# Kernel optimization log

Measured on AMD Instinct MI355X. Metric: run time of the kernel, lower is better.

The kernel has to match this reference:

```python
import jax, jax.numpy as jnp
import numpy as np

N, F, H, T = 100000, 128, 128, 10
E = 1600000
NUM_GRAPHS = 512
BN_EPS = 1e-5


def setup_inputs() -> dict:
    key = jax.random.key(0)
    ks = jax.random.split(key, 16)
    x = jax.random.normal(ks[0], (N, F), dtype=jnp.float32)
    edge_index = jax.random.randint(ks[1], (2, E), 0, N, dtype=jnp.int64)
    batch = jnp.sort(jax.random.randint(ks[2], (N,), 0, NUM_GRAPHS, dtype=jnp.int64))
    s = lambda fin: 1.0 / np.sqrt(fin)
    return {
        "x": x, "edge_index": edge_index, "batch": batch,
        # GINConv 1 MLP: Linear(F,H) -> BN(H) -> ReLU -> Linear(H,H)
        "W1a": jax.random.uniform(ks[3], (F, H), jnp.float32, -s(F), s(F)),
        "b1a": jax.random.uniform(ks[4], (H,), jnp.float32, -s(F), s(F)),
        "g1": jnp.ones((H,), jnp.float32),
        "bt1": jnp.zeros((H,), jnp.float32),
        "W1b": jax.random.uniform(ks[5], (H, H), jnp.float32, -s(H), s(H)),
        "b1b": jax.random.uniform(ks[6], (H,), jnp.float32, -s(H), s(H)),
        # GINConv 2 MLP
        "W2a": jax.random.uniform(ks[7], (H, H), jnp.float32, -s(H), s(H)),
        "b2a": jax.random.uniform(ks[8], (H,), jnp.float32, -s(H), s(H)),
        "g2": jnp.ones((H,), jnp.float32),
        "bt2": jnp.zeros((H,), jnp.float32),
        "W2b": jax.random.uniform(ks[9], (H, H), jnp.float32, -s(H), s(H)),
        "b2b": jax.random.uniform(ks[10], (H,), jnp.float32, -s(H), s(H)),
        # final Linear(H, T)
        "Wl": jax.random.uniform(ks[11], (H, T), jnp.float32, -s(H), s(H)),
        "bl": jax.random.uniform(ks[12], (T,), jnp.float32, -s(H), s(H)),
    }


def _batchnorm(h, gamma, beta):
    # training-mode BN over the node dimension (biased variance), eps=1e-5
    mean = jnp.mean(h, axis=0)
    var = jnp.mean(jnp.square(h - mean), axis=0)
    return (h - mean) * jax.lax.rsqrt(var + BN_EPS) * gamma + beta


def _gin_conv(x, edge_index, Wa, ba, gamma, beta, Wb, bb):
    src, dst = edge_index[0], edge_index[1]
    # sum-aggregate neighbor messages: scatter-add x[src] into dst rows
    agg = jax.ops.segment_sum(x[src], dst, num_segments=x.shape[0])
    h = (x + agg) @ Wa + ba          # eps=0 in GINConv default
    h = jax.nn.relu(_batchnorm(h, gamma, beta))
    return h @ Wb + bb


def reference(x, edge_index, batch, W1a, b1a, g1, bt1, W1b, b1b,
              W2a, b2a, g2, bt2, W2b, b2b, Wl, bl):
    h = jax.nn.relu(_gin_conv(x, edge_index, W1a, b1a, g1, bt1, W1b, b1b))
    h = jax.nn.relu(_gin_conv(h, edge_index, W2a, b2a, g2, bt2, W2b, b2b))
    pooled = jax.ops.segment_sum(h, batch, num_segments=NUM_GRAPHS)  # [G, H]
    return pooled @ Wl + bl  # [G, T]
```

## Files before the change

### kernel.cpp

```cpp
#include <hip/hip_runtime.h>
#include <cstdint>
#include <cstddef>

#define NFEAT 128
#define TGRAPH 10
#define NGRAPHS 512
#define BN_EPS 1e-5f
#define BIN_CHUNK 2048

typedef __attribute__((ext_vector_type(8))) short bf16x8;
typedef __attribute__((ext_vector_type(4))) float f32x4;

__device__ __forceinline__ float bf2f(short s) {
    union { unsigned u; float f; } c;
    c.u = ((unsigned)(unsigned short)s) << 16;
    return c.f;
}
__device__ __forceinline__ short f2bf(float f) {
    union { float f; unsigned u; } c;
    c.f = f;
    unsigned u = c.u;
    return (short)((u + 0x7fffu + ((u >> 16) & 1u)) >> 16);
}

__global__ __launch_bounds__(256) void k_bucket_hist(const int* __restrict__ dst,
                                                     int* __restrict__ bhist, int E) {
    __shared__ int h[256];
    int t = threadIdx.x;
    h[t] = 0;
    __syncthreads();
    for (int e = blockIdx.x * blockDim.x + t; e < E; e += gridDim.x * blockDim.x)
        atomicAdd(&h[dst[e] >> 9], 1);
    __syncthreads();
    if (h[t]) atomicAdd(&bhist[t], h[t]);
}

__global__ void k_bucket_scan(const int* __restrict__ bhist, int* __restrict__ bbase,
                              int* __restrict__ cur256, int E) {
    __shared__ int s[256];
    int t = threadIdx.x;
    int v = bhist[t];
    s[t] = v;
    __syncthreads();
    for (int off = 1; off < 256; off <<= 1) {
        int x = 0;
        if (t >= off) x = s[t - off];
        __syncthreads();
        if (t >= off) s[t] += x;
        __syncthreads();
    }
    int excl = s[t] - v;
    bbase[t] = excl;
    cur256[t] = excl;
    if (t == 255) bbase[256] = E;
}

__global__ __launch_bounds__(256) void k_bin_scatter(const int* __restrict__ src,
                                                     const int* __restrict__ dst,
                                                     int* __restrict__ cur256,
                                                     int2* __restrict__ binned, int E) {
    __shared__ int hist[256];
    __shared__ int base[256];
    int t = threadIdx.x;
    int e0 = blockIdx.x * BIN_CHUNK;
    int e1 = min(e0 + BIN_CHUNK, E);
    hist[t] = 0;
    __syncthreads();
    for (int e = e0 + t; e < e1; e += 256) {
        int b = dst[e] >> 9;
        atomicAdd(&hist[b], 1);
    }
    __syncthreads();
    int c = hist[t];
    if (c > 0) base[t] = atomicAdd(&cur256[t], c);
    __syncthreads();
    hist[t] = 0;
    __syncthreads();
    for (int e = e0 + t; e < e1; e += 256) {
        int d = dst[e];
        int b = d >> 9;
        int loc = atomicAdd(&hist[b], 1);
        binned[base[b] + loc] = make_int2(src[e], d);
    }
}

__global__ __launch_bounds__(512) void k_bucket_csr(const int2* __restrict__ binned,
                                                    const int* __restrict__ bbase,
                                                    int* __restrict__ rowptr,
                                                    int* __restrict__ adj,
                                                    int N, int E, int nb) {
    __shared__ int deg[512];
    __shared__ int cur[512];
    int b = blockIdx.x;
    int t = threadIdx.x;
    int e0 = bbase[b], e1 = bbase[b + 1];
    deg[t] = 0;
    __syncthreads();
    for (int e = e0 + t; e < e1; e += 512)
        atomicAdd(&deg[binned[e].y & 511], 1);
    __syncthreads();
    int v = deg[t];
    for (int off = 1; off < 512; off <<= 1) {
        int x = 0;
        if (t >= off) x = deg[t - off];
        __syncthreads();
        if (t >= off) deg[t] += x;
        __syncthreads();
    }
    int excl = deg[t] - v;
    cur[t] = excl;
    int node = b * 512 + t;
    if (node < N) rowptr[node] = e0 + excl;
    if (b == nb - 1 && t == 0) rowptr[N] = E;
    __syncthreads();
    for (int e = e0 + t; e < e1; e += 512) {
        int2 p = binned[e];
        int loc = atomicAdd(&cur[p.y & 511], 1);
        adj[e0 + loc] = p.x;
    }
}

__global__ void k_prep(const float* __restrict__ x, short* __restrict__ xbf,
                       const float* __restrict__ W0, const float* __restrict__ W1,
                       const float* __restrict__ W2, const float* __restrict__ W3,
                       short* __restrict__ Wf, int n4) {
    int i = blockIdx.x * blockDim.x + threadIdx.x;
    if (i < n4) {
        float4 v = ((const float4*)x)[i];
        ushort4 o;
        o.x = (unsigned short)f2bf(v.x);
        o.y = (unsigned short)f2bf(v.y);
        o.z = (unsigned short)f2bf(v.z);
        o.w = (unsigned short)f2bf(v.w);
        ((ushort4*)xbf)[i] = o;
    } else {
        int idx = i - n4;
        if (idx < 4 * 16384) {
            int w = idx >> 14, r = idx & 16383;
            int j = r & 7, lane = (r >> 3) & 63, ct = (r >> 9) & 7, kc = r >> 12;
            int k = kc * 32 + (lane >> 4) * 8 + j;
            int n = ct * 16 + (lane & 15);
            const float* W = (w == 0) ? W0 : (w == 1) ? W1 : (w == 2) ? W2 : W3;
            Wf[idx] = f2bf(W[k * NFEAT + n]);
        }
    }
}

__global__ __launch_bounds__(256) void k_aggregate_bf(const short* __restrict__ X,
                                                      const int* __restrict__ rowptr,
                                                      const int* __restrict__ adj,
                                                      short* __restrict__ XA, int N) {
    int lane = threadIdx.x & 63;
    int wid = (blockIdx.x * blockDim.x + threadIdx.x) >> 6;
    int nw = (gridDim.x * blockDim.x) >> 6;
    for (; wid < N; wid += nw) {
        unsigned sv = *(const unsigned*)(X + (size_t)wid * NFEAT + lane * 2);
        float ax = bf2f((short)(sv & 0xffff));
        float ay = bf2f((short)(sv >> 16));
        int e = rowptr[wid], r1 = rowptr[wid + 1];
        for (; e + 8 <= r1; e += 8) {
            int s[8];
#pragma unroll
            for (int j = 0; j < 8; j++) s[j] = adj[e + j];
            unsigned v[8];
#pragma unroll
            for (int j = 0; j < 8; j++)
                v[j] = *(const unsigned*)(X + (size_t)s[j] * NFEAT + lane * 2);
#pragma unroll
            for (int j = 0; j < 8; j++) {
                ax += bf2f((short)(v[j] & 0xffff));
                ay += bf2f((short)(v[j] >> 16));
            }
        }
        for (; e < r1; ++e) {
            int s0 = adj[e];
            unsigned v0 = *(const unsigned*)(X + (size_t)s0 * NFEAT + lane * 2);
            ax += bf2f((short)(v0 & 0xffff));
            ay += bf2f((short)(v0 >> 16));
        }
        unsigned o = (unsigned)(unsigned short)f2bf(ax) | ((unsigned)(unsigned short)f2bf(ay) << 16);
        *(unsigned*)(XA + (size_t)wid * NFEAT + lane * 2) = o;
    }
}

template <bool BN_RELU_IN, bool RELU_OUT, bool STATS>
__global__ __launch_bounds__(256) void k_gemm_mfma(const short* __restrict__ A,
                                                   const short* __restrict__ Wf,
                                                   const float* __restrict__ bias,
                                                   const float* __restrict__ scale,
                                                   const float* __restrict__ shift,
                                                   float* __restrict__ stats,
                                                   short* __restrict__ C, int N) {
    __shared__ float s_sum[NFEAT];
    __shared__ float s_sq[NFEAT];
    int tid = threadIdx.x;
    int wave = tid >> 6, lane = tid & 63;
    int quad = lane >> 4, l16 = lane & 15;
    int row_base = blockIdx.x * 128 + wave * 32;

    if constexpr (STATS) {
        if (tid < NFEAT) { s_sum[tid] = 0.f; s_sq[tid] = 0.f; }
        __syncthreads();
    }

    f32x4 acc[2][8];
#pragma unroll
    for (int i = 0; i < 2; i++)
#pragma unroll
        for (int j = 0; j < 8; j++) acc[i][j] = (f32x4){0.f, 0.f, 0.f, 0.f};

    int r0 = row_base + l16;
    int r1 = r0 + 16;

#pragma unroll
    for (int kc = 0; kc < 4; ++kc) {
        int koff = kc * 32 + quad * 8;
        bf16x8 a0 = {}, a1 = {};
        if (r0 < N) a0 = *(const bf16x8*)(A + (size_t)r0 * NFEAT + koff);
        if (r1 < N) a1 = *(const bf16x8*)(A + (size_t)r1 * NFEAT + koff);
        if constexpr (BN_RELU_IN) {
            float sc[8], sh[8];
            *(float4*)(sc) = *(const float4*)(scale + koff);
            *(float4*)(sc + 4) = *(const float4*)(scale + koff + 4);
            *(float4*)(sh) = *(const float4*)(shift + koff);
            *(float4*)(sh + 4) = *(const float4*)(shift + koff + 4);
#pragma unroll
            for (int j = 0; j < 8; j++) {
                float v = fmaxf(bf2f(a0[j]) * sc[j] + sh[j], 0.f);
                float u = fmaxf(bf2f(a1[j]) * sc[j] + sh[j], 0.f);
                a0[j] = f2bf(v);
                a1[j] = f2bf(u);
            }
        }
        const short* wp = Wf + ((size_t)(kc * 8) * 64 + lane) * 8;
#pragma unroll
        for (int ct = 0; ct < 8; ++ct) {
            bf16x8 b = *(const bf16x8*)(wp + (size_t)ct * 64 * 8);
            acc[0][ct] = __builtin_amdgcn_mfma_f32_16x16x32_bf16(a0, b, acc[0][ct], 0, 0, 0);
            acc[1][ct] = __builtin_amdgcn_mfma_f32_16x16x32_bf16(a1, b, acc[1][ct], 0, 0, 0);
        }
    }

#pragma unroll
    for (int ct = 0; ct < 8; ++ct) {
        int col = ct * 16 + l16;
        float bv = bias[col];
        float ls = 0.f, ls2 = 0.f;
#pragma unroll
        for (int rt = 0; rt < 2; ++rt) {
#pragma unroll
            for (int reg = 0; reg < 4; ++reg) {
                int row = row_base + rt * 16 + quad * 4 + reg;
                if (row < N) {
                    float v = acc[rt][ct][reg] + bv;
                    if constexpr (RELU_OUT) v = fmaxf(v, 0.f);
                    C[(size_t)row * NFEAT + col] = f2bf(v);
                    if constexpr (STATS) { ls += v; ls2 += v * v; }
                }
            }
        }
        if constexpr (STATS) {
            atomicAdd(&s_sum[col], ls);
            atomicAdd(&s_sq[col], ls2);
        }
    }

    if constexpr (STATS) {
        __syncthreads();
        if (tid < NFEAT) {
            atomicAdd(&stats[tid], s_sum[tid]);
            atomicAdd(&stats[NFEAT + tid], s_sq[tid]);
        }
    }
}

__global__ void k_bnfinalize(const float* __restrict__ stats, const float* __restrict__ gamma,
                             const float* __restrict__ beta, float* __restrict__ scale,
                             float* __restrict__ shift, int N) {
    int c = threadIdx.x;
    if (c < NFEAT) {
        float mean = stats[c] / (float)N;
        float var = stats[NFEAT + c] / (float)N - mean * mean;
        float inv = rsqrtf(var + BN_EPS);
        float sc = gamma[c] * inv;
        scale[c] = sc;
        shift[c] = beta[c] - mean * sc;
    }
}

__global__ __launch_bounds__(256) void k_pool2(const short* __restrict__ H2,
                                               const int* __restrict__ batch,
                                               float* __restrict__ pooled, int N) {
    int t = threadIdx.x;
    int c2 = t & 63;
    int rofs = t >> 6;
    int n0 = blockIdx.x * 128;
    int cur = -1;
    float ax = 0.f, ay = 0.f;
    for (int i = 0; i < 32; ++i) {
        int n = n0 + rofs + i * 4;
        if (n >= N) break;
        int g = batch[n];
        if (g != cur) {
            if (cur >= 0) {
                atomicAdd(&pooled[cur * NFEAT + c2 * 2], ax);
                atomicAdd(&pooled[cur * NFEAT + c2 * 2 + 1], ay);
            }
            cur = g; ax = 0.f; ay = 0.f;
        }
        unsigned v = *(const unsigned*)(H2 + (size_t)n * NFEAT + c2 * 2);
        ax += bf2f((short)(v & 0xffff));
        ay += bf2f((short)(v >> 16));
    }
    if (cur >= 0) {
        atomicAdd(&pooled[cur * NFEAT + c2 * 2], ax);
        atomicAdd(&pooled[cur * NFEAT + c2 * 2 + 1], ay);
    }
}

__global__ void k_final(const float* __restrict__ pooled, const float* __restrict__ Wl,
                        const float* __restrict__ bl, float* __restrict__ out) {
    int idx = blockIdx.x * blockDim.x + threadIdx.x;
    if (idx >= NGRAPHS * TGRAPH) return;
    int g = idx / TGRAPH, t = idx % TGRAPH;
    const float* p = pooled + (size_t)g * NFEAT;
    float acc = bl[t];
#pragma unroll 16
    for (int k = 0; k < NFEAT; ++k) acc += p[k] * Wl[k * TGRAPH + t];
    out[idx] = acc;
}

extern "C" void kernel_launch(void* const* d_in, const int* in_sizes, int n_in,
                              void* d_out, int out_size, void* d_ws, size_t ws_size,
                              hipStream_t stream) {
    const float* x = (const float*)d_in[0];
    const int* ei = (const int*)d_in[1];
    const int* batch = (const int*)d_in[2];
    const float* W1a = (const float*)d_in[3];
    const float* b1a = (const float*)d_in[4];
    const float* g1 = (const float*)d_in[5];
    const float* bt1 = (const float*)d_in[6];
    const float* W1b = (const float*)d_in[7];
    const float* b1b = (const float*)d_in[8];
    const float* W2a = (const float*)d_in[9];
    const float* b2a = (const float*)d_in[10];
    const float* g2 = (const float*)d_in[11];
    const float* bt2 = (const float*)d_in[12];
    const float* W2b = (const float*)d_in[13];
    const float* b2b = (const float*)d_in[14];
    const float* Wl = (const float*)d_in[15];
    const float* bl = (const float*)d_in[16];
    float* out = (float*)d_out;

    int N = in_sizes[2];
    int E = in_sizes[1] / 2;
    int nb = (N + 511) >> 9;
    const int* src = ei;
    const int* dst = ei + E;

    char* ws = (char*)d_ws;
    size_t off = 0;
    auto alloc = [&](size_t bytes) -> void* {
        void* p = ws + off;
        off = (off + bytes + 255) & ~(size_t)255;
        return p;
    };
    short* xbf = (short*)alloc((size_t)N * NFEAT * 2);
    short* ag = (short*)alloc((size_t)N * NFEAT * 2);
    short* ybf = (short*)alloc((size_t)N * NFEAT * 2);
    short* hbf = (short*)alloc((size_t)N * NFEAT * 2);
    short* h2bf = (short*)alloc((size_t)N * NFEAT * 2);
    short* Wf = (short*)alloc((size_t)4 * 16384 * 2);
    int* adj = (int*)alloc((size_t)E * 4);
    int2* binned = (int2*)alloc((size_t)E * 8);
    int* rowptr = (int*)alloc((size_t)(N + 1) * 4);
    int* bbase = (int*)alloc(257 * 4);
    int* cur256 = (int*)alloc(256 * 4);
    float* scale = (float*)alloc(128 * 4);
    float* shift = (float*)alloc(128 * 4);
    int* bhist = (int*)alloc(256 * 4);
    float* stats1 = (float*)alloc(256 * 4);
    float* stats2 = (float*)alloc(256 * 4);
    float* pooled = (float*)alloc((size_t)NGRAPHS * NFEAT * 4);
    size_t zbytes = (char*)(pooled + (size_t)NGRAPHS * NFEAT) - (char*)bhist;

    hipMemsetAsync(bhist, 0, zbytes, stream);

    k_bucket_hist<<<784, 256, 0, stream>>>(dst, bhist, E);
    k_bucket_scan<<<1, 256, 0, stream>>>(bhist, bbase, cur256, E);
    k_bin_scatter<<<(E + BIN_CHUNK - 1) / BIN_CHUNK, 256, 0, stream>>>(src, dst, cur256, binned, E);
    k_bucket_csr<<<nb, 512, 0, stream>>>(binned, bbase, rowptr, adj, N, E, nb);

    int n4 = N * NFEAT / 4;
    int prepTot = n4 + 4 * 16384;
    k_prep<<<(prepTot + 255) / 256, 256, 0, stream>>>(x, xbf, W1a, W1b, W2a, W2b, Wf, n4);

    int gemmBlocks = (N + 127) / 128;

    k_aggregate_bf<<<2048, 256, 0, stream>>>(xbf, rowptr, adj, ag, N);
    k_gemm_mfma<false, false, true><<<gemmBlocks, 256, 0, stream>>>(ag, Wf + 0 * 16384, b1a, nullptr, nullptr, stats1, ybf, N);
    k_bnfinalize<<<1, 128, 0, stream>>>(stats1, g1, bt1, scale, shift, N);
    k_gemm_mfma<true, true, false><<<gemmBlocks, 256, 0, stream>>>(ybf, Wf + 1 * 16384, b1b, scale, shift, nullptr, hbf, N);

    k_aggregate_bf<<<2048, 256, 0, stream>>>(hbf, rowptr, adj, ag, N);
    k_gemm_mfma<false, false, true><<<gemmBlocks, 256, 0, stream>>>(ag, Wf + 2 * 16384, b2a, nullptr, nullptr, stats2, ybf, N);
    k_bnfinalize<<<1, 128, 0, stream>>>(stats2, g2, bt2, scale, shift, N);
    k_gemm_mfma<true, true, false><<<gemmBlocks, 256, 0, stream>>>(ybf, Wf + 3 * 16384, b2b, scale, shift, nullptr, h2bf, N);

    k_pool2<<<(N + 127) / 128, 256, 0, stream>>>(h2bf, batch, pooled, N);
    k_final<<<(NGRAPHS * TGRAPH + 255) / 256, 256, 0, stream>>>(pooled, Wl, bl, out);
}
```

Baseline: 537.0 us.

## Slice feature columns across blocks and parallelize neighbor edges within a wave

Rewrites the neighbor aggregation so each block handles one 32-byte slice of the feature row, and each wave splits its lanes into 8 edge slots by 8 feature lanes. Neighbor partial sums are then combined with cross-lane shuffles. This is meant to raise memory-level parallelism per node and to improve cache locality, since each block only touches one eighth of the feature matrix. The cost is 8x redundant rowptr/adj reads and narrow 32-byte gathers per edge, plus idle slots on nodes with few neighbors.

After: 916.6 us. 70.7% more time.

```diff
diff --git a/kernel.cpp b/kernel.cpp
--- a/kernel.cpp
+++ b/kernel.cpp
@@ -146,40 +146,46 @@
     }
 }
 
-__global__ __launch_bounds__(256) void k_aggregate_bf(const short* __restrict__ X,
+__global__ __launch_bounds__(256) void k_aggregate_sl(const short* __restrict__ X,
                                                       const int* __restrict__ rowptr,
                                                       const int* __restrict__ adj,
                                                       short* __restrict__ XA, int N) {
-    int lane = threadIdx.x & 63;
-    int wid = (blockIdx.x * blockDim.x + threadIdx.x) >> 6;
-    int nw = (gridDim.x * blockDim.x) >> 6;
-    for (; wid < N; wid += nw) {
-        unsigned sv = *(const unsigned*)(X + (size_t)wid * NFEAT + lane * 2);
-        float ax = bf2f((short)(sv & 0xffff));
-        float ay = bf2f((short)(sv >> 16));
-        int e = rowptr[wid], r1 = rowptr[wid + 1];
-        for (; e + 8 <= r1; e += 8) {
-            int s[8];
-#pragma unroll
-            for (int j = 0; j < 8; j++) s[j] = adj[e + j];
-            unsigned v[8];
-#pragma unroll
-            for (int j = 0; j < 8; j++)
-                v[j] = *(const unsigned*)(X + (size_t)s[j] * NFEAT + lane * 2);
-#pragma unroll
-            for (int j = 0; j < 8; j++) {
-                ax += bf2f((short)(v[j] & 0xffff));
-                ay += bf2f((short)(v[j] >> 16));
+    int tid = threadIdx.x;
+    int lane = tid & 63;
+    int slot = lane >> 3;
+    int d = lane & 7;
+    int slice = blockIdx.x & 7;
+    int sliceByte = slice * 32 + d * 4;
+    int wid = (blockIdx.x >> 3) * 4 + (tid >> 6);
+    int nw = (gridDim.x >> 3) * 4;
+    const char* Xb = (const char*)X;
+    for (int n = wid; n < N; n += nw) {
+        int r0 = rowptr[n], r1 = rowptr[n + 1];
+        float ax = 0.f, ay = 0.f;
+        for (int e = r0; e < r1; e += 8) {
+            int ee = e + slot;
+            unsigned v = 0;
+            if (ee < r1) {
+                int srow = adj[ee];
+                v = *(const unsigned*)(Xb + (size_t)srow * 256 + sliceByte);
             }
-        }
-        for (; e < r1; ++e) {
-            int s0 = adj[e];
-            unsigned v0 = *(const unsigned*)(X + (size_t)s0 * NFEAT + lane * 2);
-            ax += bf2f((short)(v0 & 0xffff));
-            ay += bf2f((short)(v0 >> 16));
-        }
-        unsigned o = (unsigned)(unsigned short)f2bf(ax) | ((unsigned)(unsigned short)f2bf(ay) << 16);
-        *(unsigned*)(XA + (size_t)wid * NFEAT + lane * 2) = o;
+            ax += bf2f((short)(v & 0xffff));
+            ay += bf2f((short)(v >> 16));
+        }
+        ax += __shfl_xor(ax, 8);
+        ay += __shfl_xor(ay, 8);
+        ax += __shfl_xor(ax, 16);
+        ay += __shfl_xor(ay, 16);
+        ax += __shfl_xor(ax, 32);
+        ay += __shfl_xor(ay, 32);
+        if (slot == 0) {
+            unsigned sv = *(const unsigned*)(Xb + (size_t)n * 256 + sliceByte);
+            ax += bf2f((short)(sv & 0xffff));
+            ay += bf2f((short)(sv >> 16));
+            unsigned o = (unsigned)(unsigned short)f2bf(ax) |
+                         ((unsigned)(unsigned short)f2bf(ay) << 16);
+            *(unsigned*)((char*)XA + (size_t)n * 256 + sliceByte) = o;
+        }
     }
 }
 
@@ -396,13 +402,14 @@
     k_prep<<<(prepTot + 255) / 256, 256, 0, stream>>>(x, xbf, W1a, W1b, W2a, W2b, Wf, n4);
 
     int gemmBlocks = (N + 127) / 128;
-
-    k_aggregate_bf<<<2048, 256, 0, stream>>>(xbf, rowptr, adj, ag, N);
+    int aggBlocks = 8 * 512;
+
+    k_aggregate_sl<<<aggBlocks, 256, 0, stream>>>(xbf, rowptr, adj, ag, N);
     k_gemm_mfma<false, false, true><<<gemmBlocks, 256, 0, stream>>>(ag, Wf + 0 * 16384, b1a, nullptr, nullptr, stats1, ybf, N);
     k_bnfinalize<<<1, 128, 0, stream>>>(stats1, g1, bt1, scale, shift, N);
     k_gemm_mfma<true, true, false><<<gemmBlocks, 256, 0, stream>>>(ybf, Wf + 1 * 16384, b1b, scale, shift, nullptr, hbf, N);
 
-    k_aggregate_bf<<<2048, 256, 0, stream>>>(hbf, rowptr, adj, ag, N);
+    k_aggregate_sl<<<aggBlocks, 256, 0, stream>>>(hbf, rowptr, adj, ag, N);
     k_gemm_mfma<false, false, true><<<gemmBlocks, 256, 0, stream>>>(ag, Wf + 2 * 16384, b2a, nullptr, nullptr, stats2, ybf, N);
     k_bnfinalize<<<1, 128, 0, stream>>>(stats2, g2, bt2, scale, shift, N);
     k_gemm_mfma<true, true, false><<<gemmBlocks, 256, 0, stream>>>(ybf, Wf + 3 * 16384, b2b, scale, shift, nullptr, h2bf, N);
```

## Split each node's gather across four 16-lane groups with 16-byte loads

Applied to the files above, without the earlier changes.

The aggregation kernel now assigns four edge streams per wave. Each 16-lane group loads a full 256-byte bf16 row with uint4 loads, and partial sums are combined with cross-lane shuffles. It replaces the grid-stride loop with one wave per node and uses a cheaper bf16-to-float unpack. The goal is more independent loads in flight and wider memory transactions for the irregular neighbor gather. In exchange it uses more registers for the eight accumulators and adds shuffle overhead, and three quarters of the lanes sit idle during the final store.

Measured after the change: 530.6 us. No clear change (-1.2%).

```diff
diff --git a/kernel.cpp b/kernel.cpp
--- a/kernel.cpp
+++ b/kernel.cpp
@@ -21,6 +21,13 @@
     c.f = f;
     unsigned u = c.u;
     return (short)((u + 0x7fffu + ((u >> 16) & 1u)) >> 16);
+}
+__device__ __forceinline__ void acc2(float& a, float& b, unsigned v) {
+    union { unsigned u; float f; } lo, hi;
+    lo.u = v << 16;
+    hi.u = v & 0xffff0000u;
+    a += lo.f;
+    b += hi.f;
 }
 
 __global__ __launch_bounds__(256) void k_bucket_hist(const int* __restrict__ dst,
@@ -146,40 +153,52 @@
     }
 }
 
-__global__ __launch_bounds__(256) void k_aggregate_bf(const short* __restrict__ X,
+__global__ __launch_bounds__(256) void k_aggregate_v4(const short* __restrict__ X,
                                                       const int* __restrict__ rowptr,
                                                       const int* __restrict__ adj,
                                                       short* __restrict__ XA, int N) {
-    int lane = threadIdx.x & 63;
-    int wid = (blockIdx.x * blockDim.x + threadIdx.x) >> 6;
-    int nw = (gridDim.x * blockDim.x) >> 6;
-    for (; wid < N; wid += nw) {
-        unsigned sv = *(const unsigned*)(X + (size_t)wid * NFEAT + lane * 2);
-        float ax = bf2f((short)(sv & 0xffff));
-        float ay = bf2f((short)(sv >> 16));
-        int e = rowptr[wid], r1 = rowptr[wid + 1];
-        for (; e + 8 <= r1; e += 8) {
-            int s[8];
-#pragma unroll
-            for (int j = 0; j < 8; j++) s[j] = adj[e + j];
-            unsigned v[8];
-#pragma unroll
-            for (int j = 0; j < 8; j++)
-                v[j] = *(const unsigned*)(X + (size_t)s[j] * NFEAT + lane * 2);
-#pragma unroll
-            for (int j = 0; j < 8; j++) {
-                ax += bf2f((short)(v[j] & 0xffff));
-                ay += bf2f((short)(v[j] >> 16));
-            }
-        }
-        for (; e < r1; ++e) {
-            int s0 = adj[e];
-            unsigned v0 = *(const unsigned*)(X + (size_t)s0 * NFEAT + lane * 2);
-            ax += bf2f((short)(v0 & 0xffff));
-            ay += bf2f((short)(v0 >> 16));
-        }
-        unsigned o = (unsigned)(unsigned short)f2bf(ax) | ((unsigned)(unsigned short)f2bf(ay) << 16);
-        *(unsigned*)(XA + (size_t)wid * NFEAT + lane * 2) = o;
+    int tid = threadIdx.x;
+    int lane = tid & 63;
+    int g = lane >> 4;
+    int p = lane & 15;
+    int wid = (blockIdx.x * blockDim.x + tid) >> 6;
+    if (wid >= N) return;
+    const uint4* Xv = (const uint4*)X;
+    float acc[8];
+#pragma unroll
+    for (int j = 0; j < 8; j++) acc[j] = 0.f;
+    int r0 = rowptr[wid], r1 = rowptr[wid + 1];
+    for (int e = r0; e < r1; e += 8) {
+        int e0 = e + g, e1 = e + 4 + g;
+        uint4 v0 = {0u, 0u, 0u, 0u}, v1 = {0u, 0u, 0u, 0u};
+        if (e0 < r1) v0 = Xv[(size_t)adj[e0] * 16 + p];
+        if (e1 < r1) v1 = Xv[(size_t)adj[e1] * 16 + p];
+        acc2(acc[0], acc[1], v0.x);
+        acc2(acc[2], acc[3], v0.y);
+        acc2(acc[4], acc[5], v0.z);
+        acc2(acc[6], acc[7], v0.w);
+        acc2(acc[0], acc[1], v1.x);
+        acc2(acc[2], acc[3], v1.y);
+        acc2(acc[4], acc[5], v1.z);
+        acc2(acc[6], acc[7], v1.w);
+    }
+#pragma unroll
+    for (int j = 0; j < 8; j++) {
+        acc[j] += __shfl_xor(acc[j], 16);
+        acc[j] += __shfl_xor(acc[j], 32);
+    }
+    if (g == 0) {
+        uint4 sv = Xv[(size_t)wid * 16 + p];
+        acc2(acc[0], acc[1], sv.x);
+        acc2(acc[2], acc[3], sv.y);
+        acc2(acc[4], acc[5], sv.z);
+        acc2(acc[6], acc[7], sv.w);
+        uint4 o;
+        o.x = (unsigned)(unsigned short)f2bf(acc[0]) | ((unsigned)(unsigned short)f2bf(acc[1]) << 16);
+        o.y = (unsigned)(unsigned short)f2bf(acc[2]) | ((unsigned)(unsigned short)f2bf(acc[3]) << 16);
+        o.z = (unsigned)(unsigned short)f2bf(acc[4]) | ((unsigned)(unsigned short)f2bf(acc[5]) << 16);
+        o.w = (unsigned)(unsigned short)f2bf(acc[6]) | ((unsigned)(unsigned short)f2bf(acc[7]) << 16);
+        ((uint4*)XA)[(size_t)wid * 16 + p] = o;
     }
 }
 
@@ -396,13 +415,14 @@
     k_prep<<<(prepTot + 255) / 256, 256, 0, stream>>>(x, xbf, W1a, W1b, W2a, W2b, Wf, n4);
 
     int gemmBlocks = (N + 127) / 128;
-
-    k_aggregate_bf<<<2048, 256, 0, stream>>>(xbf, rowptr, adj, ag, N);
+    int aggBlocks = (N + 3) / 4;
+
+    k_aggregate_v4<<<aggBlocks, 256, 0, stream>>>(xbf, rowptr, adj, ag, N);
     k_gemm_mfma<false, false, true><<<gemmBlocks, 256, 0, stream>>>(ag, Wf + 0 * 16384, b1a, nullptr, nullptr, stats1, ybf, N);
     k_bnfinalize<<<1, 128, 0, stream>>>(stats1, g1, bt1, scale, shift, N);
     k_gemm_mfma<true, true, false><<<gemmBlocks, 256, 0, stream>>>(ybf, Wf + 1 * 16384, b1b, scale, shift, nullptr, hbf, N);
 
-    k_aggregate_bf<<<2048, 256, 0, stream>>>(hbf, rowptr, adj, ag, N);
+    k_aggregate_v4<<<aggBlocks, 256, 0, stream>>>(hbf, rowptr, adj, ag, N);
     k_gemm_mfma<false, false, true><<<gemmBlocks, 256, 0, stream>>>(ag, Wf + 2 * 16384, b2a, nullptr, nullptr, stats2, ybf, N);
     k_bnfinalize<<<1, 128, 0, stream>>>(stats2, g2, bt2, scale, shift, N);
     k_gemm_mfma<true, true, false><<<gemmBlocks, 256, 0, stream>>>(ybf, Wf + 3 * 16384, b2b, scale, shift, nullptr, h2bf, N);
```
